# Optimization experiments

Measured on AMD Instinct MI355X. Metric: run time of the kernel, lower is better.

Reference implementation:

```python
import jax, jax.numpy as jnp
import numpy as np

R = 4
D = 2 * R + 1  # 9
B, C, H, W = 1, 256, 48, 96


def setup_inputs() -> dict:
    key = jax.random.key(0)
    k1, k2, k3, k4, k5 = jax.random.split(key, 5)
    f1 = jax.random.normal(k1, (B, C, H, W), dtype=jnp.float32)
    f2 = jax.random.normal(k2, (B, C, H, W), dtype=jnp.float32)
    cx = jax.random.uniform(k3, (B, H, W), dtype=jnp.float32) * (W - 1)
    cy = jax.random.uniform(k4, (B, H, W), dtype=jnp.float32) * (H - 1)
    coords = jnp.stack([cx, cy], axis=1)  # (B,2,H,W), ch0=x, ch1=y
    # DAP: 1x1 conv over (2r+1)^2 channels, identity init (perturbed so it is non-trivial)
    w_dap = jnp.eye(D * D, dtype=jnp.float32) + 0.02 * jax.random.normal(k5, (D * D, D * D), dtype=jnp.float32)
    return {"f1": f1, "f2": f2, "coords": coords, "w_dap": w_dap}


def _bilinear_sample(img, px, py):
    # img: (C,H,W); px,py: (M,) pixel coords; zeros padding, align_corners=True semantics
    c, h, w = img.shape
    x0 = jnp.floor(px)
    y0 = jnp.floor(py)
    x1 = x0 + 1.0
    y1 = y0 + 1.0
    wx1 = px - x0
    wx0 = 1.0 - wx1
    wy1 = py - y0
    wy0 = 1.0 - wy1
    flat = img.reshape(c, h * w)

    def corner(xi, yi, wgt):
        valid = (xi >= 0) & (xi <= w - 1) & (yi >= 0) & (yi <= h - 1)
        xc = jnp.clip(xi, 0, w - 1).astype(jnp.int32)
        yc = jnp.clip(yi, 0, h - 1).astype(jnp.int32)
        v = flat[:, yc * w + xc]  # (C,M)
        return v * (wgt * valid.astype(wgt.dtype))[None, :]

    return (corner(x0, y0, wx0 * wy0) + corner(x1, y0, wx1 * wy0)
            + corner(x0, y1, wx0 * wy1) + corner(x1, y1, wx1 * wy1))


def _corr_forward(f1, f2, coords, w_dap):
    b, c, h, w = f1.shape
    d = jnp.linspace(-R, R, D, dtype=f1.dtype)
    # centroids[b, i, y, j, x] = (coords_x + dx[i], coords_y + dy[j])
    px = coords[:, 0][:, None, :, None, :] + d[None, :, None, None, None]  # (B,D,H,1,W)->(B,D,H,D,W)
    py = coords[:, 1][:, None, :, None, :] + d[None, None, None, :, None]
    px = jnp.broadcast_to(px, (b, D, h, D, w)).reshape(b, -1)
    py = jnp.broadcast_to(py, (b, D, h, D, w)).reshape(b, -1)
    samp = jax.vmap(_bilinear_sample)(f2, px, py)  # (B, C, D*H*D*W)
    f2s = samp.reshape(b, c, D, h, D, w)
    corr = jnp.einsum('bcihjw,bchw->bijhw', f2s, f1) / jnp.sqrt(jnp.asarray(c, f1.dtype))
    cf = corr.reshape(b, D * D, h, w)
    out = jnp.einsum('od,bdhw->bohw', w_dap, cf)  # DAP 1x1 conv, no bias
    return out  # (B, (2r+1)^2, H, W)


def reference(f1, f2, coords, w_dap):
    return _corr_forward(f1, f2, coords, w_dap)
```

## Files before the change

### kernel.cpp

```cpp
#include <hip/hip_runtime.h>

#define HH   48
#define WW   96
#define CC   256
#define RRAD 4
#define DD   9
#define DD2  81
#define PP   10
#define HWSZ (HH * WW)
#define ROWB 512
#define ZOFF ((unsigned)HWSZ * ROWB)

typedef __attribute__((ext_vector_type(8))) short short8v;
typedef __attribute__((ext_vector_type(4))) float f32x4;

__device__ __forceinline__ unsigned bf16rne(float f) {
  unsigned u = __float_as_uint(f);
  return (u + 0x7FFFu + ((u >> 16) & 1u)) >> 16;
}

__device__ __forceinline__ void gload_lds16(const char* g, char* l) {
  __builtin_amdgcn_global_load_lds(
      (const __attribute__((address_space(1))) char*)g,
      (__attribute__((address_space(3))) char*)l, 16, 0, 0);
}

__global__ __launch_bounds__(256) void transpose_to_bf16(
    const float* __restrict__ f1, const float* __restrict__ f2,
    const float* __restrict__ w_dap, char* __restrict__ f2tb,
    char* __restrict__ f1tb, char* __restrict__ zpage,
    unsigned short* __restrict__ Wf) {
  __shared__ float tile[64][65];
  const float* src = (blockIdx.y == 0) ? f1 : f2;
  char* dst = (blockIdx.y == 0) ? f1tb : f2tb;

  const int tid = threadIdx.x;
  if (blockIdx.y == 0 && blockIdx.x == 0 && tid < 32) {
    float4 z = {0.f, 0.f, 0.f, 0.f};
    *(float4*)(zpage + tid * 16) = z;
  }
  if (blockIdx.y == 0 && blockIdx.x < 36) {
    int gid = blockIdx.x * 256 + tid;
    int g = gid >> 9;
    int idx = gid & 511;
    int ln = idx >> 3, e = idx & 7;
    int m = g / 3, kt = g - m * 3;
    int r = m * 16 + (ln & 15);
    int c = kt * 32 + (ln >> 4) * 8 + e;
    float v = (r < DD2 && c < DD2) ? w_dap[r * DD2 + c] : 0.f;
    Wf[gid] = (unsigned short)bf16rne(v);
  }

  const int tiles_p = HWSZ / 64;
  const int bc = blockIdx.x / tiles_p;
  const int bp = blockIdx.x % tiles_p;
  const int c0 = bc * 64, p0 = bp * 64;

#pragma unroll
  for (int k = 0; k < 16; k++) {
    int idx = k * 256 + tid;
    int cl = idx >> 6, pl = idx & 63;
    tile[cl][pl] = src[(size_t)(c0 + cl) * HWSZ + p0 + pl];
  }
  __syncthreads();
#pragma unroll
  for (int k = 0; k < 8; k++) {
    int idx = k * 256 + tid;
    int pl = idx >> 5, cp = idx & 31;
    unsigned lo = bf16rne(tile[2 * cp][pl]);
    unsigned hi = bf16rne(tile[2 * cp + 1][pl]);
    *(unsigned*)(dst + (size_t)(p0 + pl) * ROWB + (size_t)c0 * 2 + cp * 4) =
        lo | (hi << 16);
  }
}

__global__ __launch_bounds__(256, 3) void corr_main(
    const char* __restrict__ f2tb, const char* __restrict__ f1tb,
    const float* __restrict__ coords, const unsigned short* __restrict__ Wf,
    float* __restrict__ out) {
  __shared__ __align__(16) char patch[100 * ROWB];
  __shared__ __align__(16) char f1buf[1024];
  __shared__ float dots[112];
  __shared__ __align__(16) unsigned short cb[96];

  const int p = blockIdx.x;
  const int tid = threadIdx.x;
  const int lane = tid & 63, wid = tid >> 6;
  const int hi = lane >> 4, lo = lane & 15;
  const int sub = lane >> 5;
  const char* zp = f2tb + ZOFF;

  const float cx = coords[p];
  const float cy = coords[HWSZ + p];
  const float fxf = floorf(cx), fyf = floorf(cy);
  const float fx = cx - fxf, fy = cy - fyf;
  const int xb = (int)fxf - RRAD;
  const int yb = (int)fyf - RRAD;

  {
    const char* fs = (lane < 32) ? (f1tb + (size_t)p * ROWB + (lane & 31) * 16)
                                 : (zp + (lane & 31) * 16);
    gload_lds16(fs, f1buf);
  }
#pragma unroll
  for (int half = 0; half < 2; half++) {
    const int ti = wid + half * 4;
    if (ti < 7) {
#pragma unroll
      for (int rp = 0; rp < 8; rp++) {
        const int base = ti * 16 + rp * 2;
        if (base < 100) {
          const int r = base + sub;
          const int yy = (r * 205) >> 11;
          const int xx = r - yy * 10;
          const int gy = yb + yy, gx = xb + xx;
          const unsigned ro = (gx >= 0 && gx < WW && gy >= 0 && gy < HH)
                                  ? (unsigned)(gy * WW + gx) * ROWB : ZOFF;
          const char* src =
              f2tb + ro + (((lane & 31) * 16) ^ ((r & 7) << 4));
          gload_lds16(src, &patch[base * ROWB]);
        }
      }
    }
  }

  if (wid == 3)      asm volatile("s_waitcnt vmcnt(0)" ::: "memory");
  else if (wid == 2) asm volatile("s_waitcnt vmcnt(2)" ::: "memory");
  else               asm volatile("s_waitcnt vmcnt(8)" ::: "memory");
  __builtin_amdgcn_sched_barrier(0);

  short8v bfrag[8];
#pragma unroll
  for (int kt = 0; kt < 8; kt++)
    bfrag[kt] = *(const short8v*)(f1buf + hi * 16 + kt * 64);

  {
    const int m = wid;
    int row = m * 16 + lo;
    const char* rp2 = patch + row * ROWB;
    const int swz = (row & 7) << 4;
    short8v a[8];
#pragma unroll
    for (int kt = 0; kt < 8; kt++)
      a[kt] = *(const short8v*)(rp2 + ((hi * 16 + kt * 64) ^ swz));
    f32x4 acc = {0.f, 0.f, 0.f, 0.f};
#pragma unroll
    for (int kt = 0; kt < 8; kt++)
      acc = __builtin_amdgcn_mfma_f32_16x16x32_bf16(a[kt], bfrag[kt], acc, 0, 0, 0);
    if (lo == 0) {
      const int rb = m * 16 + hi * 4;
      dots[rb + 0] = acc[0]; dots[rb + 1] = acc[1];
      dots[rb + 2] = acc[2]; dots[rb + 3] = acc[3];
    }
  }

  if (wid < 3) {
    asm volatile("s_waitcnt vmcnt(0)" ::: "memory");
    __builtin_amdgcn_sched_barrier(0);
    const int m = wid + 4;
    int row = m * 16 + lo;
    row = row > 99 ? 99 : row;
    const char* rp2 = patch + row * ROWB;
    const int swz = (row & 7) << 4;
    short8v a[8];
#pragma unroll
    for (int kt = 0; kt < 8; kt++)
      a[kt] = *(const short8v*)(rp2 + ((hi * 16 + kt * 64) ^ swz));
    f32x4 acc = {0.f, 0.f, 0.f, 0.f};
#pragma unroll
    for (int kt = 0; kt < 8; kt++)
      acc = __builtin_amdgcn_mfma_f32_16x16x32_bf16(a[kt], bfrag[kt], acc, 0, 0, 0);
    if (lo == 0) {
      const int rb = m * 16 + hi * 4;
      dots[rb + 0] = acc[0]; dots[rb + 1] = acc[1];
      dots[rb + 2] = acc[2]; dots[rb + 3] = acc[3];
    }
  }

  asm volatile("s_waitcnt lgkmcnt(0)" ::: "memory");
  __builtin_amdgcn_s_barrier();

  if (tid < 96) {
    float c = 0.f;
    if (tid < DD2) {
      const int i = tid / DD, j = tid - i * DD;
      const float d00 = dots[j * PP + i];
      const float d01 = dots[j * PP + i + 1];
      const float d10 = dots[(j + 1) * PP + i];
      const float d11 = dots[(j + 1) * PP + i + 1];
      c = ((1.f - fy) * ((1.f - fx) * d00 + fx * d01) +
           fy * ((1.f - fx) * d10 + fx * d11)) * 0.0625f;
    }
    cb[tid] = (unsigned short)bf16rne(c);
  }
  asm volatile("s_waitcnt lgkmcnt(0)" ::: "memory");
  __builtin_amdgcn_s_barrier();

  short8v bq[3];
#pragma unroll
  for (int kt = 0; kt < 3; kt++)
    bq[kt] = *(const short8v*)&cb[kt * 32 + hi * 8];
#pragma unroll
  for (int mi = 0; mi < 2; mi++) {
    const int m = wid + mi * 4;
    if (m < 6) {
      const unsigned short* wr = Wf + ((size_t)(m * 3) * 64 + lane) * 8;
      f32x4 acc = {0.f, 0.f, 0.f, 0.f};
#pragma unroll
      for (int kt = 0; kt < 3; kt++) {
        short8v aw = *(const short8v*)(wr + (size_t)kt * 512);
        acc = __builtin_amdgcn_mfma_f32_16x16x32_bf16(aw, bq[kt], acc, 0, 0, 0);
      }
      if (lo == 0) {
#pragma unroll
        for (int j = 0; j < 4; j++) {
          const int o = m * 16 + hi * 4 + j;
          if (o < DD2) out[(size_t)o * HWSZ + p] = acc[j];
        }
      }
    }
  }
}

extern "C" void kernel_launch(void* const* d_in, const int* in_sizes, int n_in,
                              void* d_out, int out_size, void* d_ws, size_t ws_size,
                              hipStream_t stream) {
  const float* f1     = (const float*)d_in[0];
  const float* f2     = (const float*)d_in[1];
  const float* coords = (const float*)d_in[2];
  const float* w_dap  = (const float*)d_in[3];
  float* out = (float*)d_out;

  char* f2tb  = (char*)d_ws;
  char* zpage = f2tb + (size_t)HWSZ * ROWB;
  char* f1tb  = zpage + 512;
  unsigned short* Wf = (unsigned short*)(f1tb + (size_t)HWSZ * ROWB);

  dim3 tgrid((CC / 64) * (HWSZ / 64), 2);
  transpose_to_bf16<<<tgrid, 256, 0, stream>>>(f1, f2, w_dap, f2tb, f1tb, zpage, Wf);

  corr_main<<<dim3(HWSZ), 256, 0, stream>>>(f2tb, f1tb, coords, Wf, out);
}
```

Baseline: 35.62 us.

## Split DAP 1x1 conv into separate batched MFMA kernel over 16 pixels

```diff
diff --git a/kernel.cpp b/kernel.cpp
--- a/kernel.cpp
+++ b/kernel.cpp
@@ -76,12 +76,10 @@
 
 __global__ __launch_bounds__(256, 3) void corr_main(
     const char* __restrict__ f2tb, const char* __restrict__ f1tb,
-    const float* __restrict__ coords, const unsigned short* __restrict__ Wf,
-    float* __restrict__ out) {
+    const float* __restrict__ coords, unsigned short* __restrict__ cbg) {
   __shared__ __align__(16) char patch[100 * ROWB];
   __shared__ __align__(16) char f1buf[1024];
   __shared__ float dots[112];
-  __shared__ __align__(16) unsigned short cb[96];
 
   const int p = blockIdx.x;
   const int tid = threadIdx.x;
@@ -191,33 +189,41 @@
       c = ((1.f - fy) * ((1.f - fx) * d00 + fx * d01) +
            fy * ((1.f - fx) * d10 + fx * d11)) * 0.0625f;
     }
-    cb[tid] = (unsigned short)bf16rne(c);
-  }
-  asm volatile("s_waitcnt lgkmcnt(0)" ::: "memory");
-  __builtin_amdgcn_s_barrier();
+    cbg[(size_t)p * 96 + tid] = (unsigned short)bf16rne(c);
+  }
+}
+
+__global__ __launch_bounds__(64) void dap_gemm(
+    const unsigned short* __restrict__ cbg, const unsigned short* __restrict__ Wf,
+    float* __restrict__ out) {
+  const int lane = threadIdx.x;
+  const int hi = lane >> 4, lo = lane & 15;
+  const int p0 = blockIdx.x * 16;
 
   short8v bq[3];
 #pragma unroll
   for (int kt = 0; kt < 3; kt++)
-    bq[kt] = *(const short8v*)&cb[kt * 32 + hi * 8];
-#pragma unroll
-  for (int mi = 0; mi < 2; mi++) {
-    const int m = wid + mi * 4;
-    if (m < 6) {
-      const unsigned short* wr = Wf + ((size_t)(m * 3) * 64 + lane) * 8;
-      f32x4 acc = {0.f, 0.f, 0.f, 0.f};
-#pragma unroll
-      for (int kt = 0; kt < 3; kt++) {
-        short8v aw = *(const short8v*)(wr + (size_t)kt * 512);
-        acc = __builtin_amdgcn_mfma_f32_16x16x32_bf16(aw, bq[kt], acc, 0, 0, 0);
-      }
-      if (lo == 0) {
-#pragma unroll
-        for (int j = 0; j < 4; j++) {
-          const int o = m * 16 + hi * 4 + j;
-          if (o < DD2) out[(size_t)o * HWSZ + p] = acc[j];
-        }
-      }
+    bq[kt] = *(const short8v*)(cbg + (size_t)(p0 + lo) * 96 + kt * 32 + hi * 8);
+
+  f32x4 acc[6];
+#pragma unroll
+  for (int m = 0; m < 6; m++) acc[m] = (f32x4){0.f, 0.f, 0.f, 0.f};
+
+#pragma unroll
+  for (int m = 0; m < 6; m++) {
+#pragma unroll
+    for (int kt = 0; kt < 3; kt++) {
+      short8v aw = *(const short8v*)(Wf + ((size_t)(m * 3 + kt) * 64 + lane) * 8);
+      acc[m] = __builtin_amdgcn_mfma_f32_16x16x32_bf16(aw, bq[kt], acc[m], 0, 0, 0);
+    }
+  }
+
+#pragma unroll
+  for (int m = 0; m < 6; m++) {
+#pragma unroll
+    for (int j = 0; j < 4; j++) {
+      const int o = m * 16 + hi * 4 + j;
+      if (o < DD2) out[(size_t)o * HWSZ + p0 + lo] = acc[m][j];
     }
   }
 }
@@ -234,10 +240,13 @@
   char* f2tb  = (char*)d_ws;
   char* zpage = f2tb + (size_t)HWSZ * ROWB;
   char* f1tb  = zpage + 512;
-  unsigned short* Wf = (unsigned short*)(f1tb + (size_t)HWSZ * ROWB);
+  unsigned short* Wf  = (unsigned short*)(f1tb + (size_t)HWSZ * ROWB);
+  unsigned short* cbg = Wf + 9216;
 
   dim3 tgrid((CC / 64) * (HWSZ / 64), 2);
   transpose_to_bf16<<<tgrid, 256, 0, stream>>>(f1, f2, w_dap, f2tb, f1tb, zpage, Wf);
 
-  corr_main<<<dim3(HWSZ), 256, 0, stream>>>(f2tb, f1tb, coords, Wf, out);
-}
+  corr_main<<<dim3(HWSZ), 256, 0, stream>>>(f2tb, f1tb, coords, cbg);
+
+  dap_gemm<<<dim3(HWSZ / 16), 64, 0, stream>>>(cbg, Wf, out);
+}
```

Result: faster. 33.53 us (-5.9%).
